# Kernel tuning notes

Hardware: AMD Instinct MI355X
Metric: run time of the kernel (lower is better)

## Reference

```python
import jax, jax.numpy as jnp
import numpy as np

N = 1024
H = 128

def setup_inputs() -> dict:
    key = jax.random.key(0)
    ks = jax.random.split(key, 16)
    s = 1.0 / np.sqrt(H)
    inp = {
        "h": jax.random.normal(ks[0], (N, H), jnp.float32),
        "x": jax.random.normal(ks[1], (N, 2), jnp.float32),
        "batch": jnp.zeros((N,), jnp.int64),
        # Linear params stored as [in, out]
        "Wq": jax.random.normal(ks[2], (H, H), jnp.float32) * s,
        "bq": jnp.zeros((H,), jnp.float32),
        "Wk": jax.random.normal(ks[3], (H, H), jnp.float32) * s,
        "bk": jnp.zeros((H,), jnp.float32),
        "Wv": jax.random.normal(ks[4], (H, H), jnp.float32) * s,
        "bv": jnp.zeros((H,), jnp.float32),
        "We1": jax.random.normal(ks[5], (2, H), jnp.float32) * (1.0 / np.sqrt(2.0)),
        "be1": jnp.zeros((H,), jnp.float32),
        "We2": jax.random.normal(ks[6], (H, H), jnp.float32) * s,
        "be2": jnp.zeros((H,), jnp.float32),
        "Wc": jax.random.normal(ks[7], (H, 1), jnp.float32) * s,
        "bc": jnp.zeros((1,), jnp.float32),
    }
    return inp

def reference(h, x, batch, Wq, bq, Wk, bk, Wv, bv, We1, be1, We2, be2, Wc, bc):
    hidden = h.shape[-1]
    # pairwise relative coordinates: [N, N, 2]
    rel_x = x[:, None, :] - x[None, :, :]
    # edge MLP: Linear(2->H) -> ReLU -> Linear(H->H), [N, N, H]
    edge_feat = jax.nn.relu(rel_x @ We1 + be1) @ We2 + be2
    # attention: scaled dot-product over all pairs
    q = h @ Wq + bq
    k = h @ Wk + bk
    v = h @ Wv + bv
    attn_score = (q @ k.T) / jnp.sqrt(jnp.asarray(hidden, h.dtype))  # [N, N]
    attn_weight = jax.nn.softmax(attn_score, axis=-1)
    agg_h = attn_weight @ v  # [N, H]
    # coordinate update: per-pair scalar gate times rel_x, attn-weighted sum over j
    gate = edge_feat @ Wc + bc                     # [N, N, 1]
    delta_x = jnp.sum(attn_weight[:, :, None] * gate * rel_x, axis=1)  # [N, 2]
    return (h + agg_h, x + delta_x)
```

## Files before the change

### kernel.cpp

```cpp
#include <hip/hip_runtime.h>
#include <math.h>

#define NN 1024
#define HH 128

typedef _Float16 h2 __attribute__((ext_vector_type(2)));
typedef _Float16 h4 __attribute__((ext_vector_type(4)));

__device__ inline float fdot2(h2 a, h2 b, float c) {
  return __builtin_amdgcn_fdot2(a, b, c, false);
}

__global__ __launch_bounds__(384) void qkv_kernel(
    const float* __restrict__ h,
    const float* __restrict__ Wq, const float* __restrict__ bq,
    const float* __restrict__ Wk, const float* __restrict__ bk,
    const float* __restrict__ Wv, const float* __restrict__ bv,
    const float* __restrict__ We2, const float* __restrict__ be2,
    const float* __restrict__ Wc, const float* __restrict__ bc,
    float* __restrict__ q, h2* __restrict__ kTp, h2* __restrict__ vp,
    float* __restrict__ Wc2, float* __restrict__ bc2) {
  const int t = threadIdx.x;

  if (blockIdx.x == 256) {
    if (t < HH) {
      float a = 0.f;
      for (int d = 0; d < HH; ++d) a = fmaf(We2[t * HH + d], Wc[d], a);
      Wc2[t] = a;
      if (t == 0) {
        float b = bc[0];
        for (int d = 0; d < HH; ++d) b = fmaf(be2[d], Wc[d], b);
        *bc2 = b;
      }
    }
    return;
  }

  __shared__ float4 hs4[HH];
  const int r0 = blockIdx.x * 4;
  if (t < HH) {
    hs4[t] = make_float4(h[(r0 + 0) * HH + t], h[(r0 + 1) * HH + t],
                         h[(r0 + 2) * HH + t], h[(r0 + 3) * HH + t]);
  }
  __syncthreads();

  const int mat = t >> 7;
  const int col = t & 127;
  const float* W = (mat == 0) ? Wq : (mat == 1) ? Wk : Wv;
  const float* B = (mat == 0) ? bq : (mat == 1) ? bk : bv;
  const float b = B[col];
  float a0 = b, a1 = b, a2 = b, a3 = b;
#pragma unroll 8
  for (int c = 0; c < HH; ++c) {
    float w = W[c * HH + col];
    float4 hv = hs4[c];
    a0 = fmaf(hv.x, w, a0);
    a1 = fmaf(hv.y, w, a1);
    a2 = fmaf(hv.z, w, a2);
    a3 = fmaf(hv.w, w, a3);
  }
  if (mat == 0) {
    q[(r0 + 0) * HH + col] = a0;
    q[(r0 + 1) * HH + col] = a1;
    q[(r0 + 2) * HH + col] = a2;
    q[(r0 + 3) * HH + col] = a3;
  } else if (mat == 1) {
    _Float16* kf = (_Float16*)kTp;
    const int base = ((col >> 1) * NN + r0) * 2 + (col & 1);
    kf[base + 0] = (_Float16)a0;
    kf[base + 2] = (_Float16)a1;
    kf[base + 4] = (_Float16)a2;
    kf[base + 6] = (_Float16)a3;
  } else {
    h2 v01, v23;
    v01.x = (_Float16)a0; v01.y = (_Float16)a1;
    v23.x = (_Float16)a2; v23.y = (_Float16)a3;
    h2* e = vp + ((r0 >> 1) * HH + col);
    e[0] = v01;
    e[HH] = v23;
  }
}

__global__ __launch_bounds__(512) void attn_kernel(
    const float* __restrict__ h, const float* __restrict__ x,
    const float* __restrict__ q, const h2* __restrict__ kTp,
    const h2* __restrict__ vp,
    const float* __restrict__ We1, const float* __restrict__ be1,
    const float* __restrict__ Wc2p, const float* __restrict__ bc2p,
    float* __restrict__ out) {
  __shared__ h4 qpx[HH / 2];
  __shared__ h4 wAB[HH / 2];
  __shared__ h4 wBC[HH / 2];
  __shared__ h4 wspi[NN / 2];
  __shared__ float xs[NN * 2];
  __shared__ float part[8][2][HH];
  __shared__ float red[6][8];

  const int i0 = blockIdx.x * 2, i1 = i0 + 1;
  const int tid = threadIdx.x;
  const int lane = tid & 63, wave = tid >> 6;

  if (tid < HH / 2) {
    const int u = tid;
    h4 a, b, c;
    a[0] = (_Float16)q[i0 * HH + 2 * u];
    a[1] = (_Float16)q[i0 * HH + 2 * u + 1];
    a[2] = (_Float16)q[i1 * HH + 2 * u];
    a[3] = (_Float16)q[i1 * HH + 2 * u + 1];
    qpx[u] = a;
    b[0] = (_Float16)We1[2 * u];
    b[1] = (_Float16)We1[2 * u + 1];
    b[2] = (_Float16)We1[HH + 2 * u];
    b[3] = (_Float16)We1[HH + 2 * u + 1];
    wAB[u] = b;
    c[0] = (_Float16)be1[2 * u];
    c[1] = (_Float16)be1[2 * u + 1];
    c[2] = (_Float16)Wc2p[2 * u];
    c[3] = (_Float16)Wc2p[2 * u + 1];
    wBC[u] = c;
  }
  for (int j = tid; j < NN * 2; j += 512) xs[j] = x[j];
  const float bc2 = *bc2p;
  __syncthreads();

  const float xi0x = xs[2 * i0], xi0y = xs[2 * i0 + 1];
  const float xi1x = xs[2 * i1], xi1y = xs[2 * i1 + 1];
  const int j0 = 2 * tid, j1 = j0 + 1;
  const float xj0x = xs[2 * j0], xj0y = xs[2 * j0 + 1];
  const float xj1x = xs[2 * j1], xj1y = xs[2 * j1 + 1];
  const float rx00 = xi0x - xj0x, ry00 = xi0y - xj0y;
  const float rx01 = xi0x - xj1x, ry01 = xi0y - xj1y;
  const float rx10 = xi1x - xj0x, ry10 = xi1y - xj0y;
  const float rx11 = xi1x - xj1x, ry11 = xi1y - xj1y;

  h2 RX00, RY00, RX01, RY01, RX10, RY10, RX11, RY11, Z2;
  RX00.x = RX00.y = (_Float16)rx00;  RY00.x = RY00.y = (_Float16)ry00;
  RX01.x = RX01.y = (_Float16)rx01;  RY01.x = RY01.y = (_Float16)ry01;
  RX10.x = RX10.y = (_Float16)rx10;  RY10.x = RY10.y = (_Float16)ry10;
  RX11.x = RX11.y = (_Float16)rx11;  RY11.x = RY11.y = (_Float16)ry11;
  Z2.x = Z2.y = (_Float16)0;

  float s00 = 0.f, s01 = 0.f, s10 = 0.f, s11 = 0.f;
  float g00 = bc2, g01 = bc2, g10 = bc2, g11 = bc2;
  const h4* kT4 = (const h4*)kTp;
#pragma unroll 4
  for (int u = 0; u < HH / 2; ++u) {
    h4 kk = kT4[u * (NN / 2) + tid];
    h4 qq = qpx[u];
    h4 ab = wAB[u];
    h4 bcv = wBC[u];
    h2 ka, kb, q0, q1, w0, w1, bb, cc;
    ka.x = kk[0]; ka.y = kk[1];
    kb.x = kk[2]; kb.y = kk[3];
    q0.x = qq[0]; q0.y = qq[1];
    q1.x = qq[2]; q1.y = qq[3];
    w0.x = ab[0]; w0.y = ab[1];
    w1.x = ab[2]; w1.y = ab[3];
    bb.x = bcv[0]; bb.y = bcv[1];
    cc.x = bcv[2]; cc.y = bcv[3];
    s00 = fdot2(q0, ka, s00);
    s01 = fdot2(q0, kb, s01);
    s10 = fdot2(q1, ka, s10);
    s11 = fdot2(q1, kb, s11);
    h2 t00 = RX00 * w0 + RY00 * w1 + bb;
    h2 t01 = RX01 * w0 + RY01 * w1 + bb;
    h2 t10 = RX10 * w0 + RY10 * w1 + bb;
    h2 t11 = RX11 * w0 + RY11 * w1 + bb;
    t00 = __builtin_elementwise_max(t00, Z2);
    t01 = __builtin_elementwise_max(t01, Z2);
    t10 = __builtin_elementwise_max(t10, Z2);
    t11 = __builtin_elementwise_max(t11, Z2);
    g00 = fdot2(t00, cc, g00);
    g01 = fdot2(t01, cc, g01);
    g10 = fdot2(t10, cc, g10);
    g11 = fdot2(t11, cc, g11);
  }
  const float scale = 0.08838834764831845f;
  const float e00 = __expf(s00 * scale), e01 = __expf(s01 * scale);
  const float e10 = __expf(s10 * scale), e11 = __expf(s11 * scale);
  {
    h4 w;
    w[0] = (_Float16)e00; w[1] = (_Float16)e01;
    w[2] = (_Float16)e10; w[3] = (_Float16)e11;
    wspi[tid] = w;
  }
  const float wg00 = e00 * g00, wg01 = e01 * g01;
  const float wg10 = e10 * g10, wg11 = e11 * g11;
  float l0 = e00 + e01, l1 = e10 + e11;
  float dx0 = fmaf(wg00, rx00, wg01 * rx01);
  float dy0 = fmaf(wg00, ry00, wg01 * ry01);
  float dx1 = fmaf(wg10, rx10, wg11 * rx11);
  float dy1 = fmaf(wg10, ry10, wg11 * ry11);
#pragma unroll
  for (int off = 32; off > 0; off >>= 1) {
    l0 += __shfl_down(l0, off);
    l1 += __shfl_down(l1, off);
    dx0 += __shfl_down(dx0, off);
    dy0 += __shfl_down(dy0, off);
    dx1 += __shfl_down(dx1, off);
    dy1 += __shfl_down(dy1, off);
  }
  if (lane == 0) {
    red[0][wave] = l0;  red[1][wave] = l1;
    red[2][wave] = dx0; red[3][wave] = dy0;
    red[4][wave] = dx1; red[5][wave] = dy1;
  }
  __syncthreads();
  float sum0 = 0.f, sum1 = 0.f;
#pragma unroll
  for (int w = 0; w < 8; ++w) { sum0 += red[0][w]; sum1 += red[1][w]; }
  const float inv0 = 1.f / sum0, inv1 = 1.f / sum1;

  if (tid == 0) {
    float DX0 = 0.f, DY0 = 0.f, DX1 = 0.f, DY1 = 0.f;
#pragma unroll
    for (int w = 0; w < 8; ++w) {
      DX0 += red[2][w]; DY0 += red[3][w];
      DX1 += red[4][w]; DY1 += red[5][w];
    }
    out[NN * HH + i0 * 2 + 0] = xi0x + DX0 * inv0;
    out[NN * HH + i0 * 2 + 1] = xi0y + DY0 * inv0;
    out[NN * HH + i1 * 2 + 0] = xi1x + DX1 * inv1;
    out[NN * HH + i1 * 2 + 1] = xi1y + DY1 * inv1;
  }

  {
    const int j2b = wave * 64;
    const h4* v4 = (const h4*)vp;
    float a0x = 0.f, a0y = 0.f, a1x = 0.f, a1y = 0.f;
#pragma unroll 4
    for (int jj = 0; jj < 64; ++jj) {
      const int j2 = j2b + jj;
      h4 vv = v4[j2 * 64 + lane];
      h4 wj = wspi[j2];
      h2 v0, v1, w0, w1;
      v0.x = vv[0]; v0.y = vv[1];
      v1.x = vv[2]; v1.y = vv[3];
      w0.x = wj[0]; w0.y = wj[1];
      w1.x = wj[2]; w1.y = wj[3];
      a0x = fdot2(w0, v0, a0x);
      a0y = fdot2(w0, v1, a0y);
      a1x = fdot2(w1, v0, a1x);
      a1y = fdot2(w1, v1, a1y);
    }
    part[wave][0][2 * lane] = a0x;
    part[wave][0][2 * lane + 1] = a0y;
    part[wave][1][2 * lane] = a1x;
    part[wave][1][2 * lane + 1] = a1y;
  }
  __syncthreads();
  if (tid < 256) {
    const int r = tid >> 7, c = tid & 127;
    float s = 0.f;
#pragma unroll
    for (int g = 0; g < 8; ++g) s += part[g][r][c];
    out[(i0 + r) * HH + c] = h[(i0 + r) * HH + c] + s * (r ? inv1 : inv0);
  }
}

extern "C" void kernel_launch(void* const* d_in, const int* in_sizes, int n_in,
                              void* d_out, int out_size, void* d_ws, size_t ws_size,
                              hipStream_t stream) {
  const float* h   = (const float*)d_in[0];
  const float* x   = (const float*)d_in[1];
  const float* Wq  = (const float*)d_in[3];
  const float* bq  = (const float*)d_in[4];
  const float* Wk  = (const float*)d_in[5];
  const float* bk  = (const float*)d_in[6];
  const float* Wv  = (const float*)d_in[7];
  const float* bv  = (const float*)d_in[8];
  const float* We1 = (const float*)d_in[9];
  const float* be1 = (const float*)d_in[10];
  const float* We2 = (const float*)d_in[11];
  const float* be2 = (const float*)d_in[12];
  const float* Wc  = (const float*)d_in[13];
  const float* bc  = (const float*)d_in[14];
  float* out = (float*)d_out;

  float* wsf = (float*)d_ws;
  float* q   = wsf;
  h2*   kTp  = (h2*)(wsf + NN * HH);
  h2*   vp   = kTp + (HH / 2) * NN;
  float* Wc2 = (float*)(vp + (NN / 2) * HH);
  float* bc2 = Wc2 + HH;

  qkv_kernel<<<257, 384, 0, stream>>>(h, Wq, bq, Wk, bk, Wv, bv, We2, be2, Wc,
                                      bc, q, kTp, vp, Wc2, bc2);
  attn_kernel<<<512, 512, 0, stream>>>(h, x, q, kTp, vp, We1, be1, Wc2, bc2,
                                       out);
}
```

Measured before the change: 109.3 us.

## Process four query rows per attention block to reuse K and V loads

Each attention block now handles four query rows instead of two, halving the grid to 256 blocks. Every K and V element loaded from global memory is reused across four rows, and the edge-MLP weights are packed into a single 8-wide shared vector. The cost is more registers per thread, a larger shared-memory partial buffer, and fewer blocks, which may leave some of the device's compute units underused.

Result: no change. 111.2 us (+1.8%).

```diff
diff --git a/kernel.cpp b/kernel.cpp
--- a/kernel.cpp
+++ b/kernel.cpp
@@ -6,6 +6,7 @@
 
 typedef _Float16 h2 __attribute__((ext_vector_type(2)));
 typedef _Float16 h4 __attribute__((ext_vector_type(4)));
+typedef _Float16 h8 __attribute__((ext_vector_type(8)));
 
 __device__ inline float fdot2(h2 a, h2 b, float c) {
   return __builtin_amdgcn_fdot2(a, b, c, false);
@@ -88,173 +89,183 @@
     const float* __restrict__ We1, const float* __restrict__ be1,
     const float* __restrict__ Wc2p, const float* __restrict__ bc2p,
     float* __restrict__ out) {
-  __shared__ h4 qpx[HH / 2];
-  __shared__ h4 wAB[HH / 2];
-  __shared__ h4 wBC[HH / 2];
-  __shared__ h4 wspi[NN / 2];
+  __shared__ h8 qpx8[HH / 2];
+  __shared__ h8 wcomb[HH / 2];
+  __shared__ h4 wsp01[NN / 2];
+  __shared__ h4 wsp23[NN / 2];
   __shared__ float xs[NN * 2];
-  __shared__ float part[8][2][HH];
-  __shared__ float red[6][8];
-
-  const int i0 = blockIdx.x * 2, i1 = i0 + 1;
+  __shared__ float part[8][4][HH];
+  __shared__ float red[12][8];
+
+  const int i0 = blockIdx.x * 4;
   const int tid = threadIdx.x;
   const int lane = tid & 63, wave = tid >> 6;
 
   if (tid < HH / 2) {
     const int u = tid;
-    h4 a, b, c;
-    a[0] = (_Float16)q[i0 * HH + 2 * u];
-    a[1] = (_Float16)q[i0 * HH + 2 * u + 1];
-    a[2] = (_Float16)q[i1 * HH + 2 * u];
-    a[3] = (_Float16)q[i1 * HH + 2 * u + 1];
-    qpx[u] = a;
-    b[0] = (_Float16)We1[2 * u];
-    b[1] = (_Float16)We1[2 * u + 1];
-    b[2] = (_Float16)We1[HH + 2 * u];
-    b[3] = (_Float16)We1[HH + 2 * u + 1];
-    wAB[u] = b;
-    c[0] = (_Float16)be1[2 * u];
-    c[1] = (_Float16)be1[2 * u + 1];
-    c[2] = (_Float16)Wc2p[2 * u];
-    c[3] = (_Float16)Wc2p[2 * u + 1];
-    wBC[u] = c;
+    h8 a, w;
+#pragma unroll
+    for (int r = 0; r < 4; ++r) {
+      a[2 * r] = (_Float16)q[(i0 + r) * HH + 2 * u];
+      a[2 * r + 1] = (_Float16)q[(i0 + r) * HH + 2 * u + 1];
+    }
+    qpx8[u] = a;
+    w[0] = (_Float16)We1[2 * u];
+    w[1] = (_Float16)We1[2 * u + 1];
+    w[2] = (_Float16)We1[HH + 2 * u];
+    w[3] = (_Float16)We1[HH + 2 * u + 1];
+    w[4] = (_Float16)be1[2 * u];
+    w[5] = (_Float16)be1[2 * u + 1];
+    w[6] = (_Float16)Wc2p[2 * u];
+    w[7] = (_Float16)Wc2p[2 * u + 1];
+    wcomb[u] = w;
   }
   for (int j = tid; j < NN * 2; j += 512) xs[j] = x[j];
   const float bc2 = *bc2p;
   __syncthreads();
 
-  const float xi0x = xs[2 * i0], xi0y = xs[2 * i0 + 1];
-  const float xi1x = xs[2 * i1], xi1y = xs[2 * i1 + 1];
-  const int j0 = 2 * tid, j1 = j0 + 1;
-  const float xj0x = xs[2 * j0], xj0y = xs[2 * j0 + 1];
-  const float xj1x = xs[2 * j1], xj1y = xs[2 * j1 + 1];
-  const float rx00 = xi0x - xj0x, ry00 = xi0y - xj0y;
-  const float rx01 = xi0x - xj1x, ry01 = xi0y - xj1y;
-  const float rx10 = xi1x - xj0x, ry10 = xi1y - xj0y;
-  const float rx11 = xi1x - xj1x, ry11 = xi1y - xj1y;
-
-  h2 RX00, RY00, RX01, RY01, RX10, RY10, RX11, RY11, Z2;
-  RX00.x = RX00.y = (_Float16)rx00;  RY00.x = RY00.y = (_Float16)ry00;
-  RX01.x = RX01.y = (_Float16)rx01;  RY01.x = RY01.y = (_Float16)ry01;
-  RX10.x = RX10.y = (_Float16)rx10;  RY10.x = RY10.y = (_Float16)ry10;
-  RX11.x = RX11.y = (_Float16)rx11;  RY11.x = RY11.y = (_Float16)ry11;
+  const float xjx0 = xs[4 * tid + 0], xjy0 = xs[4 * tid + 1];
+  const float xjx1 = xs[4 * tid + 2], xjy1 = xs[4 * tid + 3];
+  float rxf[4][2], ryf[4][2];
+  h2 RX[4][2], RY[4][2], Z2;
   Z2.x = Z2.y = (_Float16)0;
-
-  float s00 = 0.f, s01 = 0.f, s10 = 0.f, s11 = 0.f;
-  float g00 = bc2, g01 = bc2, g10 = bc2, g11 = bc2;
+#pragma unroll
+  for (int r = 0; r < 4; ++r) {
+    const float xix = xs[2 * (i0 + r)], xiy = xs[2 * (i0 + r) + 1];
+    rxf[r][0] = xix - xjx0; ryf[r][0] = xiy - xjy0;
+    rxf[r][1] = xix - xjx1; ryf[r][1] = xiy - xjy1;
+#pragma unroll
+    for (int jj = 0; jj < 2; ++jj) {
+      RX[r][jj].x = RX[r][jj].y = (_Float16)rxf[r][jj];
+      RY[r][jj].x = RY[r][jj].y = (_Float16)ryf[r][jj];
+    }
+  }
+
+  float s[4][2] = {}, g[4][2];
+#pragma unroll
+  for (int r = 0; r < 4; ++r) g[r][0] = g[r][1] = bc2;
   const h4* kT4 = (const h4*)kTp;
 #pragma unroll 4
   for (int u = 0; u < HH / 2; ++u) {
     h4 kk = kT4[u * (NN / 2) + tid];
-    h4 qq = qpx[u];
-    h4 ab = wAB[u];
-    h4 bcv = wBC[u];
-    h2 ka, kb, q0, q1, w0, w1, bb, cc;
+    h8 qq = qpx8[u];
+    h8 wc = wcomb[u];
+    h2 ka, kb, w0, w1, bb, cc;
     ka.x = kk[0]; ka.y = kk[1];
     kb.x = kk[2]; kb.y = kk[3];
-    q0.x = qq[0]; q0.y = qq[1];
-    q1.x = qq[2]; q1.y = qq[3];
-    w0.x = ab[0]; w0.y = ab[1];
-    w1.x = ab[2]; w1.y = ab[3];
-    bb.x = bcv[0]; bb.y = bcv[1];
-    cc.x = bcv[2]; cc.y = bcv[3];
-    s00 = fdot2(q0, ka, s00);
-    s01 = fdot2(q0, kb, s01);
-    s10 = fdot2(q1, ka, s10);
-    s11 = fdot2(q1, kb, s11);
-    h2 t00 = RX00 * w0 + RY00 * w1 + bb;
-    h2 t01 = RX01 * w0 + RY01 * w1 + bb;
-    h2 t10 = RX10 * w0 + RY10 * w1 + bb;
-    h2 t11 = RX11 * w0 + RY11 * w1 + bb;
-    t00 = __builtin_elementwise_max(t00, Z2);
-    t01 = __builtin_elementwise_max(t01, Z2);
-    t10 = __builtin_elementwise_max(t10, Z2);
-    t11 = __builtin_elementwise_max(t11, Z2);
-    g00 = fdot2(t00, cc, g00);
-    g01 = fdot2(t01, cc, g01);
-    g10 = fdot2(t10, cc, g10);
-    g11 = fdot2(t11, cc, g11);
+    w0.x = wc[0]; w0.y = wc[1];
+    w1.x = wc[2]; w1.y = wc[3];
+    bb.x = wc[4]; bb.y = wc[5];
+    cc.x = wc[6]; cc.y = wc[7];
+#pragma unroll
+    for (int r = 0; r < 4; ++r) {
+      h2 qr;
+      qr.x = qq[2 * r]; qr.y = qq[2 * r + 1];
+      s[r][0] = fdot2(qr, ka, s[r][0]);
+      s[r][1] = fdot2(qr, kb, s[r][1]);
+      h2 t0 = RX[r][0] * w0 + RY[r][0] * w1 + bb;
+      h2 t1 = RX[r][1] * w0 + RY[r][1] * w1 + bb;
+      t0 = __builtin_elementwise_max(t0, Z2);
+      t1 = __builtin_elementwise_max(t1, Z2);
+      g[r][0] = fdot2(t0, cc, g[r][0]);
+      g[r][1] = fdot2(t1, cc, g[r][1]);
+    }
   }
   const float scale = 0.08838834764831845f;
-  const float e00 = __expf(s00 * scale), e01 = __expf(s01 * scale);
-  const float e10 = __expf(s10 * scale), e11 = __expf(s11 * scale);
+  float e[4][2], l[4], dx[4], dy[4];
+#pragma unroll
+  for (int r = 0; r < 4; ++r) {
+    e[r][0] = __expf(s[r][0] * scale);
+    e[r][1] = __expf(s[r][1] * scale);
+    l[r] = e[r][0] + e[r][1];
+    const float wg0 = e[r][0] * g[r][0], wg1 = e[r][1] * g[r][1];
+    dx[r] = fmaf(wg0, rxf[r][0], wg1 * rxf[r][1]);
+    dy[r] = fmaf(wg0, ryf[r][0], wg1 * ryf[r][1]);
+  }
   {
-    h4 w;
-    w[0] = (_Float16)e00; w[1] = (_Float16)e01;
-    w[2] = (_Float16)e10; w[3] = (_Float16)e11;
-    wspi[tid] = w;
-  }
-  const float wg00 = e00 * g00, wg01 = e01 * g01;
-  const float wg10 = e10 * g10, wg11 = e11 * g11;
-  float l0 = e00 + e01, l1 = e10 + e11;
-  float dx0 = fmaf(wg00, rx00, wg01 * rx01);
-  float dy0 = fmaf(wg00, ry00, wg01 * ry01);
-  float dx1 = fmaf(wg10, rx10, wg11 * rx11);
-  float dy1 = fmaf(wg10, ry10, wg11 * ry11);
+    h4 wa, wb;
+    wa[0] = (_Float16)e[0][0]; wa[1] = (_Float16)e[0][1];
+    wa[2] = (_Float16)e[1][0]; wa[3] = (_Float16)e[1][1];
+    wb[0] = (_Float16)e[2][0]; wb[1] = (_Float16)e[2][1];
+    wb[2] = (_Float16)e[3][0]; wb[3] = (_Float16)e[3][1];
+    wsp01[tid] = wa;
+    wsp23[tid] = wb;
+  }
 #pragma unroll
   for (int off = 32; off > 0; off >>= 1) {
-    l0 += __shfl_down(l0, off);
-    l1 += __shfl_down(l1, off);
-    dx0 += __shfl_down(dx0, off);
-    dy0 += __shfl_down(dy0, off);
-    dx1 += __shfl_down(dx1, off);
-    dy1 += __shfl_down(dy1, off);
+#pragma unroll
+    for (int r = 0; r < 4; ++r) {
+      l[r] += __shfl_down(l[r], off);
+      dx[r] += __shfl_down(dx[r], off);
+      dy[r] += __shfl_down(dy[r], off);
+    }
   }
   if (lane == 0) {
-    red[0][wave] = l0;  red[1][wave] = l1;
-    red[2][wave] = dx0; red[3][wave] = dy0;
-    red[4][wave] = dx1; red[5][wave] = dy1;
+#pragma unroll
+    for (int r = 0; r < 4; ++r) {
+      red[r][wave] = l[r];
+      red[4 + r][wave] = dx[r];
+      red[8 + r][wave] = dy[r];
+    }
   }
   __syncthreads();
-  float sum0 = 0.f, sum1 = 0.f;
-#pragma unroll
-  for (int w = 0; w < 8; ++w) { sum0 += red[0][w]; sum1 += red[1][w]; }
-  const float inv0 = 1.f / sum0, inv1 = 1.f / sum1;
-
-  if (tid == 0) {
-    float DX0 = 0.f, DY0 = 0.f, DX1 = 0.f, DY1 = 0.f;
-#pragma unroll
-    for (int w = 0; w < 8; ++w) {
-      DX0 += red[2][w]; DY0 += red[3][w];
-      DX1 += red[4][w]; DY1 += red[5][w];
-    }
-    out[NN * HH + i0 * 2 + 0] = xi0x + DX0 * inv0;
-    out[NN * HH + i0 * 2 + 1] = xi0y + DY0 * inv0;
-    out[NN * HH + i1 * 2 + 0] = xi1x + DX1 * inv1;
-    out[NN * HH + i1 * 2 + 1] = xi1y + DY1 * inv1;
+  float inv[4];
+#pragma unroll
+  for (int r = 0; r < 4; ++r) {
+    float sum = 0.f;
+#pragma unroll
+    for (int w = 0; w < 8; ++w) sum += red[r][w];
+    inv[r] = 1.f / sum;
+  }
+  if (tid < 4) {
+    const int r = tid;
+    float DX = 0.f, DY = 0.f;
+#pragma unroll
+    for (int w = 0; w < 8; ++w) { DX += red[4 + r][w]; DY += red[8 + r][w]; }
+    out[NN * HH + (i0 + r) * 2 + 0] = xs[2 * (i0 + r)] + DX * inv[r];
+    out[NN * HH + (i0 + r) * 2 + 1] = xs[2 * (i0 + r) + 1] + DY * inv[r];
   }
 
   {
     const int j2b = wave * 64;
     const h4* v4 = (const h4*)vp;
-    float a0x = 0.f, a0y = 0.f, a1x = 0.f, a1y = 0.f;
+    float acc[4][2] = {};
 #pragma unroll 4
     for (int jj = 0; jj < 64; ++jj) {
       const int j2 = j2b + jj;
       h4 vv = v4[j2 * 64 + lane];
-      h4 wj = wspi[j2];
-      h2 v0, v1, w0, w1;
+      h4 wa = wsp01[j2];
+      h4 wb = wsp23[j2];
+      h2 v0, v1;
       v0.x = vv[0]; v0.y = vv[1];
       v1.x = vv[2]; v1.y = vv[3];
-      w0.x = wj[0]; w0.y = wj[1];
-      w1.x = wj[2]; w1.y = wj[3];
-      a0x = fdot2(w0, v0, a0x);
-      a0y = fdot2(w0, v1, a0y);
-      a1x = fdot2(w1, v0, a1x);
-      a1y = fdot2(w1, v1, a1y);
-    }
-    part[wave][0][2 * lane] = a0x;
-    part[wave][0][2 * lane + 1] = a0y;
-    part[wave][1][2 * lane] = a1x;
-    part[wave][1][2 * lane + 1] = a1y;
+      h2 w0, w1, w2, w3;
+      w0.x = wa[0]; w0.y = wa[1];
+      w1.x = wa[2]; w1.y = wa[3];
+      w2.x = wb[0]; w2.y = wb[1];
+      w3.x = wb[2]; w3.y = wb[3];
+      acc[0][0] = fdot2(w0, v0, acc[0][0]);
+      acc[0][1] = fdot2(w0, v1, acc[0][1]);
+      acc[1][0] = fdot2(w1, v0, acc[1][0]);
+      acc[1][1] = fdot2(w1, v1, acc[1][1]);
+      acc[2][0] = fdot2(w2, v0, acc[2][0]);
+      acc[2][1] = fdot2(w2, v1, acc[2][1]);
+      acc[3][0] = fdot2(w3, v0, acc[3][0]);
+      acc[3][1] = fdot2(w3, v1, acc[3][1]);
+    }
+#pragma unroll
+    for (int r = 0; r < 4; ++r) {
+      part[wave][r][2 * lane] = acc[r][0];
+      part[wave][r][2 * lane + 1] = acc[r][1];
+    }
   }
   __syncthreads();
-  if (tid < 256) {
+  {
     const int r = tid >> 7, c = tid & 127;
-    float s = 0.f;
-#pragma unroll
-    for (int g = 0; g < 8; ++g) s += part[g][r][c];
-    out[(i0 + r) * HH + c] = h[(i0 + r) * HH + c] + s * (r ? inv1 : inv0);
+    float sacc = 0.f;
+#pragma unroll
+    for (int gg = 0; gg < 8; ++gg) sacc += part[gg][r][c];
+    out[(i0 + r) * HH + c] = h[(i0 + r) * HH + c] + sacc * inv[r];
   }
 }
 
@@ -286,6 +297,6 @@
 
   qkv_kernel<<<257, 384, 0, stream>>>(h, Wq, bq, Wk, bk, Wv, bv, We2, be2, Wc,
                                       bc, q, kTp, vp, Wc2, bc2);
-  attn_kernel<<<512, 512, 0, stream>>>(h, x, q, kTp, vp, We1, be1, Wc2, bc2,
+  attn_kernel<<<256, 512, 0, stream>>>(h, x, q, kTp, vp, We1, be1, Wc2, bc2,
                                        out);
 }
```
